# Kernel optimization log

Hardware: AMD Instinct MI355X
Metric: run time of the kernel (lower is better)

## Reference

```python
import jax, jax.numpy as jnp
import numpy as np

N = 170000          # n_users + n_entities
NNZ = 2720000       # edges in sparse A_in (avg degree 16)
DIMS = [64, 64, 32, 16]
NEG_SLOPE = 0.01    # nn.LeakyReLU default
EPS = 1e-12         # F.normalize eps


def setup_inputs() -> dict:
    key = jax.random.key(0)
    ks = jax.random.split(key, 20)
    inp = {
        "embeddings": jax.random.normal(ks[0], (N, DIMS[0]), jnp.float32) * 0.1,
        "a_vals": jax.random.uniform(ks[1], (NNZ,), jnp.float32) / 16.0,  # ~row-normalized
    }
    # bi-interaction layer params, stored (in, out) so y = x @ W + b
    i = 2
    for l in range(3):
        din, dout = DIMS[l], DIMS[l + 1]
        s = 1.0 / np.sqrt(din)
        inp[f"w1_{l}"] = jax.random.normal(ks[i], (din, dout), jnp.float32) * s; i += 1
        inp[f"b1_{l}"] = jnp.zeros((dout,), jnp.float32)
        inp[f"w2_{l}"] = jax.random.normal(ks[i], (din, dout), jnp.float32) * s; i += 1
        inp[f"b2_{l}"] = jnp.zeros((dout,), jnp.float32)
    inp["a_rows"] = jax.random.randint(ks[i], (NNZ,), 0, N, jnp.int32); i += 1
    inp["a_cols"] = jax.random.randint(ks[i], (NNZ,), 0, N, jnp.int32)
    return inp


def _leaky(x):
    return jnp.where(x >= 0, x, NEG_SLOPE * x)


def _l2norm(x):
    n = jnp.sqrt(jnp.sum(x * x, axis=1, keepdims=True))
    return x / jnp.maximum(n, EPS)


def _spmm(vals, rows, cols, emb):
    # sparse A (COO) @ emb : gather source rows, scale, scatter-add to dest rows
    msgs = vals[:, None] * emb[cols]          # (nnz, d)
    return jax.ops.segment_sum(msgs, rows, num_segments=N)


def reference(embeddings, a_vals,
              w1_0, b1_0, w2_0, b2_0,
              w1_1, b1_1, w2_1, b2_1,
              w1_2, b1_2, w2_2, b2_2,
              a_rows, a_cols):
    layers = [(w1_0, b1_0, w2_0, b2_0),
              (w1_1, b1_1, w2_1, b2_1),
              (w1_2, b1_2, w2_2, b2_2)]
    ego = embeddings
    all_embed = [ego]
    for (w1, b1, w2, b2) in layers:
        side = _spmm(a_vals, a_rows, a_cols, ego)            # (N, d_in)
        sum_e = _leaky((ego + side) @ w1 + b1)               # bi-interaction
        bi_e = _leaky((ego * side) @ w2 + b2)
        ego = sum_e + bi_e                                   # dropout = identity (eval)
        all_embed.append(_l2norm(ego))
    return jnp.concatenate(all_embed, axis=1)                # (N, 176)
```

## Files before the change

### kernel.cpp

```cpp
#include <hip/hip_runtime.h>
#include <hip/hip_bf16.h>

#define NEG_SLOPE 0.01f
#define L2EPS 1e-12f
#define SCAN_CHUNK 2048
#define PART_CH 8192
#define BSHIFT 9

__device__ __forceinline__ unsigned short f2bf(float f) {
    unsigned u = __float_as_uint(f);
    return (unsigned short)((u + 0x7fffu + ((u >> 16) & 1u)) >> 16);
}


__global__ void scan_sum(const int* __restrict__ counts, int* __restrict__ partials, int n) {
    __shared__ int red[256];
    int base = blockIdx.x * SCAN_CHUNK;
    int s = 0;
    for (int i = threadIdx.x; i < SCAN_CHUNK; i += 256) {
        int idx = base + i;
        s += (idx < n) ? counts[idx] : 0;
    }
    red[threadIdx.x] = s; __syncthreads();
    for (int o = 128; o > 0; o >>= 1) {
        if (threadIdx.x < o) red[threadIdx.x] += red[threadIdx.x + o];
        __syncthreads();
    }
    if (threadIdx.x == 0) partials[blockIdx.x] = red[0];
}

__global__ void scan_partials(int* __restrict__ partials, int nb, int* __restrict__ out, int n) {
    if (threadIdx.x == 0 && blockIdx.x == 0) {
        int run = 0;
        for (int i = 0; i < nb; i++) { int v = partials[i]; partials[i] = run; run += v; }
        out[n] = run;
    }
}

__global__ void scan_apply(const int* __restrict__ counts, const int* __restrict__ partials,
                           int* __restrict__ out, int n) {
    __shared__ int lsum[256];
    int base = blockIdx.x * SCAN_CHUNK;
    int t = threadIdx.x;
    int my[8];
    int s = 0;
    int tb = base + t * 8;
    for (int i = 0; i < 8; i++) { int idx = tb + i; int v = (idx < n) ? counts[idx] : 0; my[i] = v; s += v; }
    lsum[t] = s; __syncthreads();
    for (int o = 1; o < 256; o <<= 1) {
        int v = (t >= o) ? lsum[t - o] : 0;
        __syncthreads();
        lsum[t] += v;
        __syncthreads();
    }
    int excl = lsum[t] - s + partials[blockIdx.x];
    for (int i = 0; i < 8; i++) {
        int idx = tb + i;
        if (idx < n) { out[idx] = excl; excl += my[i]; }
    }
}


__global__ void part_hist(const int* __restrict__ rows, int* __restrict__ hist,
                          int nnz, int nchunks, int B) {
    __shared__ int h[512];
    int c = blockIdx.x;
    for (int i = threadIdx.x; i < B; i += 256) h[i] = 0;
    __syncthreads();
    int s = c * PART_CH, e = min(s + PART_CH, nnz);
    for (int i = s + threadIdx.x; i < e; i += 256) atomicAdd(&h[rows[i] >> BSHIFT], 1);
    __syncthreads();
    for (int b = threadIdx.x; b < B; b += 256) hist[b * nchunks + c] = h[b];
}

__global__ void part_scatter(const int* __restrict__ rows, const int* __restrict__ cols,
                             const float* __restrict__ vals, const int* __restrict__ hscan,
                             int2* __restrict__ tmp, int nnz, int nchunks, int B) {
    __shared__ int cur[512];
    int c = blockIdx.x;
    for (int b = threadIdx.x; b < B; b += 256) cur[b] = hscan[b * nchunks + c];
    __syncthreads();
    int s = c * PART_CH, e = min(s + PART_CH, nnz);
    for (int i = s + threadIdx.x; i < e; i += 256) {
        int r = rows[i];
        int p = atomicAdd(&cur[r >> BSHIFT], 1);
        tmp[p] = make_int2(((r & 511) << 18) | cols[i], __float_as_int(vals[i]));
    }
}

__global__ void bucket_scatter(const int* __restrict__ hscan, const int2* __restrict__ tmp,
                               int2* __restrict__ pedge, int* __restrict__ offsets,
                               int nnz, int nchunks, int B, int n) {
    __shared__ int cnt[512];
    __shared__ int scn[256];
    int b = blockIdx.x;
    int t = threadIdx.x;
    int rbase = b << BSHIFT;
    cnt[t] = 0; cnt[t + 256] = 0;
    __syncthreads();
    int s = hscan[b * nchunks];
    int e = (b == B - 1) ? nnz : hscan[(b + 1) * nchunks];
    for (int j = s + t; j < e; j += 256) atomicAdd(&cnt[((unsigned)tmp[j].x) >> 18], 1);
    __syncthreads();
    int c0 = cnt[2 * t], c1 = cnt[2 * t + 1];
    int ssum = c0 + c1;
    scn[t] = ssum;
    __syncthreads();
    for (int o = 1; o < 256; o <<= 1) {
        int v = (t >= o) ? scn[t - o] : 0;
        __syncthreads();
        scn[t] += v;
        __syncthreads();
    }
    int excl = scn[t] - ssum + s;
    int g0 = rbase + 2 * t, g1 = g0 + 1;
    if (g0 < n) offsets[g0] = excl;
    if (g1 < n) offsets[g1] = excl + c0;
    cnt[2 * t] = excl;
    cnt[2 * t + 1] = excl + c0;
    if (b == B - 1 && t == 0) offsets[n] = nnz;
    __syncthreads();
    for (int j = s + t; j < e; j += 256) {
        int2 tt = tmp[j];
        int r9 = ((unsigned)tt.x) >> 18;
        int p = atomicAdd(&cnt[r9], 1);
        pedge[p] = make_int2(tt.x & 0x3FFFF, tt.y);
    }
}


__global__ void to_bf16(const float* __restrict__ src, unsigned short* __restrict__ dst, int n4) {
    int i = blockIdx.x * blockDim.x + threadIdx.x;
    if (i >= n4) return;
    float4 v = ((const float4*)src)[i];
    ushort4 o;
    o.x = f2bf(v.x); o.y = f2bf(v.y); o.z = f2bf(v.z); o.w = f2bf(v.w);
    ((ushort4*)dst)[i] = o;
}


template <int D>
__global__ void spmm_kernel(const unsigned short* __restrict__ egob, const int* __restrict__ offs,
                            const int2* __restrict__ pedge, float* __restrict__ side, int nrows) {
    constexpr int LANES = D / 8;
    int gid = blockIdx.x * blockDim.x + threadIdx.x;
    int row = gid / LANES;
    int lane = gid % LANES;
    if (row >= nrows) return;
    int j0 = offs[row], j1 = offs[row + 1];
    float acc[8] = {0.f, 0.f, 0.f, 0.f, 0.f, 0.f, 0.f, 0.f};
    for (int j = j0; j < j1; ++j) {
        int2 ed = pedge[j];
        float v = __int_as_float(ed.y);
        uint4 q = ((const uint4*)(egob + (size_t)ed.x * D))[lane];
        acc[0] += v * __uint_as_float(q.x << 16);
        acc[1] += v * __uint_as_float(q.x & 0xffff0000u);
        acc[2] += v * __uint_as_float(q.y << 16);
        acc[3] += v * __uint_as_float(q.y & 0xffff0000u);
        acc[4] += v * __uint_as_float(q.z << 16);
        acc[5] += v * __uint_as_float(q.z & 0xffff0000u);
        acc[6] += v * __uint_as_float(q.w << 16);
        acc[7] += v * __uint_as_float(q.w & 0xffff0000u);
    }
    float4* sp = (float4*)(side + (size_t)row * D + lane * 8);
    sp[0] = make_float4(acc[0], acc[1], acc[2], acc[3]);
    sp[1] = make_float4(acc[4], acc[5], acc[6], acc[7]);
}


__device__ __forceinline__ float leaky1(float x) { return x >= 0.f ? x : NEG_SLOPE * x; }

template <int DIN, int DOUT>
__global__ void dense_kernel(const float* __restrict__ ego, const float* __restrict__ side,
                             const float* __restrict__ w1, const float* __restrict__ b1,
                             const float* __restrict__ w2, const float* __restrict__ b2,
                             float* __restrict__ ego_next, unsigned short* __restrict__ egob_next,
                             float* __restrict__ outp, int col_off, int nrows) {
    constexpr int RPB = 64;
    constexpr int TX = DOUT / 4;
    constexpr int TY = 16;
    constexpr int NT = TX * TY;
    constexpr int LD4 = DIN / 4;
    constexpr int RPP = NT / LD4;

    __shared__ float sU[DIN][RPB + 4];
    __shared__ float sV[DIN][RPB + 4];
    __shared__ float sW1[DIN * DOUT];
    __shared__ float sW2[DIN * DOUT];

    int tid = threadIdx.x;
    int row0 = blockIdx.x * RPB;

    for (int i = tid; i < DIN * DOUT / 4; i += NT) {
        ((float4*)sW1)[i] = ((const float4*)w1)[i];
        ((float4*)sW2)[i] = ((const float4*)w2)[i];
    }
    {
        int kq = tid % LD4, rr = tid / LD4;
        for (int r = rr; r < RPB; r += RPP) {
            int g = row0 + r;
            if (g < nrows) {
                float4 e = ((const float4*)(ego + (size_t)g * DIN))[kq];
                float4 s = ((const float4*)(side + (size_t)g * DIN))[kq];
                sU[kq * 4 + 0][r] = e.x + s.x;
                sU[kq * 4 + 1][r] = e.y + s.y;
                sU[kq * 4 + 2][r] = e.z + s.z;
                sU[kq * 4 + 3][r] = e.w + s.w;
                sV[kq * 4 + 0][r] = e.x * s.x;
                sV[kq * 4 + 1][r] = e.y * s.y;
                sV[kq * 4 + 2][r] = e.z * s.z;
                sV[kq * 4 + 3][r] = e.w * s.w;
            }
        }
    }
    __syncthreads();

    int tx = tid % TX, ty = tid / TX;
    float4 a1[4], a2[4];
#pragma unroll
    for (int i = 0; i < 4; i++) {
        a1[i] = make_float4(0.f, 0.f, 0.f, 0.f);
        a2[i] = make_float4(0.f, 0.f, 0.f, 0.f);
    }

#pragma unroll 8
    for (int k = 0; k < DIN; k++) {
        float4 w1v = *(const float4*)&sW1[k * DOUT + tx * 4];
        float4 w2v = *(const float4*)&sW2[k * DOUT + tx * 4];
        float4 uv = *(const float4*)&sU[k][ty * 4];
        float4 vv = *(const float4*)&sV[k][ty * 4];
        a1[0].x += uv.x * w1v.x; a1[0].y += uv.x * w1v.y; a1[0].z += uv.x * w1v.z; a1[0].w += uv.x * w1v.w;
        a1[1].x += uv.y * w1v.x; a1[1].y += uv.y * w1v.y; a1[1].z += uv.y * w1v.z; a1[1].w += uv.y * w1v.w;
        a1[2].x += uv.z * w1v.x; a1[2].y += uv.z * w1v.y; a1[2].z += uv.z * w1v.z; a1[2].w += uv.z * w1v.w;
        a1[3].x += uv.w * w1v.x; a1[3].y += uv.w * w1v.y; a1[3].z += uv.w * w1v.z; a1[3].w += uv.w * w1v.w;
        a2[0].x += vv.x * w2v.x; a2[0].y += vv.x * w2v.y; a2[0].z += vv.x * w2v.z; a2[0].w += vv.x * w2v.w;
        a2[1].x += vv.y * w2v.x; a2[1].y += vv.y * w2v.y; a2[1].z += vv.y * w2v.z; a2[1].w += vv.y * w2v.w;
        a2[2].x += vv.z * w2v.x; a2[2].y += vv.z * w2v.y; a2[2].z += vv.z * w2v.z; a2[2].w += vv.z * w2v.w;
        a2[3].x += vv.w * w2v.x; a2[3].y += vv.w * w2v.y; a2[3].z += vv.w * w2v.z; a2[3].w += vv.w * w2v.w;
    }

    float4 bb1 = ((const float4*)b1)[tx];
    float4 bb2 = ((const float4*)b2)[tx];
#pragma unroll
    for (int i = 0; i < 4; i++) {
        int g = row0 + ty * 4 + i;
        float4 x;
        x.x = leaky1(a1[i].x + bb1.x) + leaky1(a2[i].x + bb2.x);
        x.y = leaky1(a1[i].y + bb1.y) + leaky1(a2[i].y + bb2.y);
        x.z = leaky1(a1[i].z + bb1.z) + leaky1(a2[i].z + bb2.z);
        x.w = leaky1(a1[i].w + bb1.w) + leaky1(a2[i].w + bb2.w);
        float ss = x.x * x.x + x.y * x.y + x.z * x.z + x.w * x.w;
#pragma unroll
        for (int o = TX >> 1; o > 0; o >>= 1) ss += __shfl_xor(ss, o, 64);
        if (g < nrows) {
            if (ego_next) {
                ((float4*)(ego_next + (size_t)g * DOUT))[tx] = x;
                ushort4 xb;
                xb.x = f2bf(x.x); xb.y = f2bf(x.y); xb.z = f2bf(x.z); xb.w = f2bf(x.w);
                ((ushort4*)(egob_next + (size_t)g * DOUT))[tx] = xb;
            }
            float inv = 1.f / fmaxf(sqrtf(ss), L2EPS);
            float4 y = make_float4(x.x * inv, x.y * inv, x.z * inv, x.w * inv);
            ((float4*)(outp + (size_t)g * 176 + col_off))[tx] = y;
        }
    }
}


__global__ void copy_embed(const float* __restrict__ emb, float* __restrict__ outp, int nrows) {
    int idx = blockIdx.x * blockDim.x + threadIdx.x;
    int total = nrows * 16;
    if (idx >= total) return;
    int row = idx >> 4, c = idx & 15;
    float4 v = ((const float4*)emb)[idx];
    ((float4*)(outp + (size_t)row * 176))[c] = v;
}

extern "C" void kernel_launch(void* const* d_in, const int* in_sizes, int n_in,
                              void* d_out, int out_size, void* d_ws, size_t ws_size,
                              hipStream_t stream) {
    const float* emb   = (const float*)d_in[0];
    const float* avals = (const float*)d_in[1];
    const float* w1_0 = (const float*)d_in[2];  const float* b1_0 = (const float*)d_in[3];
    const float* w2_0 = (const float*)d_in[4];  const float* b2_0 = (const float*)d_in[5];
    const float* w1_1 = (const float*)d_in[6];  const float* b1_1 = (const float*)d_in[7];
    const float* w2_1 = (const float*)d_in[8];  const float* b2_1 = (const float*)d_in[9];
    const float* w1_2 = (const float*)d_in[10]; const float* b1_2 = (const float*)d_in[11];
    const float* w2_2 = (const float*)d_in[12]; const float* b2_2 = (const float*)d_in[13];
    const int* arows = (const int*)d_in[14];
    const int* acols = (const int*)d_in[15];
    float* outp = (float*)d_out;

    const int N   = in_sizes[0] / 64;
    const int NNZ = in_sizes[14];

    const int B       = (N + 511) >> BSHIFT;
    const int nchunks = (NNZ + PART_CH - 1) / PART_CH;
    const int NH      = B * nchunks;

    char* w = (char*)d_ws;
    size_t off = 0;
    auto carve = [&](size_t bytes) { char* p = w + off; off += (bytes + 255) & ~(size_t)255; return p; };
    int*   offsets  = (int*)  carve((size_t)(N + 1) * 4);
    int*   partials = (int*)  carve(1024);
    int*   hist     = (int*)  carve((size_t)(NH + 1) * 4);
    int*   hscan    = (int*)  carve((size_t)(NH + 1) * 4);
    int2*  pedge    = (int2*) carve((size_t)NNZ * 8);
    float* side     = (float*)carve((size_t)N * 64 * 4);
    float* ego1     = (float*)carve((size_t)N * 64 * 4);
    float* ego2     = (float*)carve((size_t)N * 32 * 4);
    unsigned short* egob = (unsigned short*)carve((size_t)N * 64 * 2);
    int2*  tmp      = (int2*)side;

    const int NB2 = (NH + SCAN_CHUNK - 1) / SCAN_CHUNK;

    part_hist<<<nchunks, 256, 0, stream>>>(arows, hist, NNZ, nchunks, B);
    scan_sum<<<NB2, 256, 0, stream>>>(hist, partials, NH);
    scan_partials<<<1, 64, 0, stream>>>(partials, NB2, hscan, NH);
    scan_apply<<<NB2, 256, 0, stream>>>(hist, partials, hscan, NH);
    part_scatter<<<nchunks, 256, 0, stream>>>(arows, acols, avals, hscan, tmp, NNZ, nchunks, B);
    bucket_scatter<<<B, 256, 0, stream>>>(hscan, tmp, pedge, offsets, NNZ, nchunks, B, N);

    to_bf16<<<(N * 16 + 255) / 256, 256, 0, stream>>>(emb, egob, N * 16);
    copy_embed<<<(N * 16 + 255) / 256, 256, 0, stream>>>(emb, outp, N);

    const int DB = (N + 63) / 64;

    spmm_kernel<64><<<((size_t)N * 8 + 255) / 256, 256, 0, stream>>>(egob, offsets, pedge, side, N);
    dense_kernel<64, 64><<<DB, 256, 0, stream>>>(emb, side, w1_0, b1_0, w2_0, b2_0, ego1, egob, outp, 64, N);
    spmm_kernel<64><<<((size_t)N * 8 + 255) / 256, 256, 0, stream>>>(egob, offsets, pedge, side, N);
    dense_kernel<64, 32><<<DB, 128, 0, stream>>>(ego1, side, w1_1, b1_1, w2_1, b2_1, ego2, egob, outp, 128, N);
    spmm_kernel<32><<<((size_t)N * 4 + 255) / 256, 256, 0, stream>>>(egob, offsets, pedge, side, N);
    dense_kernel<32, 16><<<DB, 64, 0, stream>>>(ego2, side, w1_2, b1_2, w2_2, b2_2, nullptr, nullptr, outp, 160, N);
}
```

Baseline: 662.7 us.

## Fuse SpMM gather into dense bi-interaction layer kernel with ping-pong bf16 buffers

Each layer's sparse gather-accumulate now happens inside the dense kernel: four threads per row gather bf16 neighbor rows into registers, then write ego+side and ego*side straight into shared memory. This removes the fp32 side buffer's global write and read and three kernel launches. The bf16 copy and the embedding output copy are merged into one prep kernel, and weights are read from global or cache instead of being staged in shared memory. Two bf16 buffers alternate between layers so a layer never overwrites rows it is still reading. The trade-off is that gather parallelism drops to 256 threads per 64-row block, and load imbalance across rows can stall the GEMM phase.

```diff
diff --git a/kernel.cpp b/kernel.cpp
--- a/kernel.cpp
+++ b/kernel.cpp
@@ -129,121 +129,145 @@
 }
 
 
-__global__ void to_bf16(const float* __restrict__ src, unsigned short* __restrict__ dst, int n4) {
-    int i = blockIdx.x * blockDim.x + threadIdx.x;
-    if (i >= n4) return;
-    float4 v = ((const float4*)src)[i];
+__global__ void embed_prep(const float* __restrict__ emb, unsigned short* __restrict__ egob,
+                           float* __restrict__ outp, int nrows) {
+    int idx = blockIdx.x * blockDim.x + threadIdx.x;
+    if (idx >= nrows * 16) return;
+    int row = idx >> 4, c = idx & 15;
+    float4 v = ((const float4*)emb)[idx];
+    ((float4*)(outp + (size_t)row * 176))[c] = v;
     ushort4 o;
     o.x = f2bf(v.x); o.y = f2bf(v.y); o.z = f2bf(v.z); o.w = f2bf(v.w);
-    ((ushort4*)dst)[i] = o;
-}
-
-
-template <int D>
-__global__ void spmm_kernel(const unsigned short* __restrict__ egob, const int* __restrict__ offs,
-                            const int2* __restrict__ pedge, float* __restrict__ side, int nrows) {
-    constexpr int LANES = D / 8;
-    int gid = blockIdx.x * blockDim.x + threadIdx.x;
-    int row = gid / LANES;
-    int lane = gid % LANES;
-    if (row >= nrows) return;
-    int j0 = offs[row], j1 = offs[row + 1];
-    float acc[8] = {0.f, 0.f, 0.f, 0.f, 0.f, 0.f, 0.f, 0.f};
-    for (int j = j0; j < j1; ++j) {
-        int2 ed = pedge[j];
-        float v = __int_as_float(ed.y);
-        uint4 q = ((const uint4*)(egob + (size_t)ed.x * D))[lane];
-        acc[0] += v * __uint_as_float(q.x << 16);
-        acc[1] += v * __uint_as_float(q.x & 0xffff0000u);
-        acc[2] += v * __uint_as_float(q.y << 16);
-        acc[3] += v * __uint_as_float(q.y & 0xffff0000u);
-        acc[4] += v * __uint_as_float(q.z << 16);
-        acc[5] += v * __uint_as_float(q.z & 0xffff0000u);
-        acc[6] += v * __uint_as_float(q.w << 16);
-        acc[7] += v * __uint_as_float(q.w & 0xffff0000u);
-    }
-    float4* sp = (float4*)(side + (size_t)row * D + lane * 8);
-    sp[0] = make_float4(acc[0], acc[1], acc[2], acc[3]);
-    sp[1] = make_float4(acc[4], acc[5], acc[6], acc[7]);
+    ((ushort4*)egob)[idx] = o;
 }
 
 
 __device__ __forceinline__ float leaky1(float x) { return x >= 0.f ? x : NEG_SLOPE * x; }
 
+__device__ __forceinline__ void fma8(float v, uint4 qv, float* acc) {
+    acc[0] += v * __uint_as_float(qv.x << 16);
+    acc[1] += v * __uint_as_float(qv.x & 0xffff0000u);
+    acc[2] += v * __uint_as_float(qv.y << 16);
+    acc[3] += v * __uint_as_float(qv.y & 0xffff0000u);
+    acc[4] += v * __uint_as_float(qv.z << 16);
+    acc[5] += v * __uint_as_float(qv.z & 0xffff0000u);
+    acc[6] += v * __uint_as_float(qv.w << 16);
+    acc[7] += v * __uint_as_float(qv.w & 0xffff0000u);
+}
+
 template <int DIN, int DOUT>
-__global__ void dense_kernel(const float* __restrict__ ego, const float* __restrict__ side,
-                             const float* __restrict__ w1, const float* __restrict__ b1,
-                             const float* __restrict__ w2, const float* __restrict__ b2,
-                             float* __restrict__ ego_next, unsigned short* __restrict__ egob_next,
-                             float* __restrict__ outp, int col_off, int nrows) {
+__global__ __launch_bounds__(256, 4)
+void fused_layer(const unsigned short* __restrict__ egob, const int* __restrict__ offs,
+                 const int2* __restrict__ pedge, const float* __restrict__ ego,
+                 const float* __restrict__ w1, const float* __restrict__ b1,
+                 const float* __restrict__ w2, const float* __restrict__ b2,
+                 float* __restrict__ ego_next, unsigned short* __restrict__ egob_next,
+                 float* __restrict__ outp, int col_off, int nrows) {
     constexpr int RPB = 64;
-    constexpr int TX = DOUT / 4;
-    constexpr int TY = 16;
-    constexpr int NT = TX * TY;
-    constexpr int LD4 = DIN / 4;
-    constexpr int RPP = NT / LD4;
+    constexpr int CPL = DIN / 4;
+    constexpr int U4  = CPL / 8;
+    constexpr int TX  = DOUT / 4;
+    constexpr int TY  = 256 / TX;
+    constexpr int RPT = RPB / TY;
 
     __shared__ float sU[DIN][RPB + 4];
     __shared__ float sV[DIN][RPB + 4];
-    __shared__ float sW1[DIN * DOUT];
-    __shared__ float sW2[DIN * DOUT];
 
     int tid = threadIdx.x;
     int row0 = blockIdx.x * RPB;
 
-    for (int i = tid; i < DIN * DOUT / 4; i += NT) {
-        ((float4*)sW1)[i] = ((const float4*)w1)[i];
-        ((float4*)sW2)[i] = ((const float4*)w2)[i];
-    }
     {
-        int kq = tid % LD4, rr = tid / LD4;
-        for (int r = rr; r < RPB; r += RPP) {
-            int g = row0 + r;
-            if (g < nrows) {
-                float4 e = ((const float4*)(ego + (size_t)g * DIN))[kq];
-                float4 s = ((const float4*)(side + (size_t)g * DIN))[kq];
-                sU[kq * 4 + 0][r] = e.x + s.x;
-                sU[kq * 4 + 1][r] = e.y + s.y;
-                sU[kq * 4 + 2][r] = e.z + s.z;
-                sU[kq * 4 + 3][r] = e.w + s.w;
-                sV[kq * 4 + 0][r] = e.x * s.x;
-                sV[kq * 4 + 1][r] = e.y * s.y;
-                sV[kq * 4 + 2][r] = e.z * s.z;
-                sV[kq * 4 + 3][r] = e.w * s.w;
+        int r = tid >> 2, q = tid & 3;
+        int g = row0 + r;
+        float acc[CPL];
+#pragma unroll
+        for (int i = 0; i < CPL; i++) acc[i] = 0.f;
+        if (g < nrows) {
+            int j0 = offs[g], j1 = offs[g + 1];
+            int j = j0;
+            for (; j + 1 < j1; j += 2) {
+                int2 e0 = pedge[j];
+                int2 e1 = pedge[j + 1];
+                float v0 = __int_as_float(e0.y);
+                float v1 = __int_as_float(e1.y);
+                const uint4* s0 = (const uint4*)(egob + (size_t)e0.x * DIN) + q * U4;
+                const uint4* s1 = (const uint4*)(egob + (size_t)e1.x * DIN) + q * U4;
+                uint4 qa[U4], qb[U4];
+#pragma unroll
+                for (int u = 0; u < U4; u++) qa[u] = s0[u];
+#pragma unroll
+                for (int u = 0; u < U4; u++) qb[u] = s1[u];
+#pragma unroll
+                for (int u = 0; u < U4; u++) fma8(v0, qa[u], acc + u * 8);
+#pragma unroll
+                for (int u = 0; u < U4; u++) fma8(v1, qb[u], acc + u * 8);
             }
+            if (j < j1) {
+                int2 e0 = pedge[j];
+                float v0 = __int_as_float(e0.y);
+                const uint4* s0 = (const uint4*)(egob + (size_t)e0.x * DIN) + q * U4;
+                uint4 qa[U4];
+#pragma unroll
+                for (int u = 0; u < U4; u++) qa[u] = s0[u];
+#pragma unroll
+                for (int u = 0; u < U4; u++) fma8(v0, qa[u], acc + u * 8);
+            }
+            const float4* ep = (const float4*)(ego + (size_t)g * DIN) + q * (CPL / 4);
+#pragma unroll
+            for (int i = 0; i < CPL / 4; i++) {
+                float4 e = ep[i];
+                int k0 = q * CPL + i * 4;
+                sU[k0 + 0][r] = e.x + acc[i * 4 + 0]; sV[k0 + 0][r] = e.x * acc[i * 4 + 0];
+                sU[k0 + 1][r] = e.y + acc[i * 4 + 1]; sV[k0 + 1][r] = e.y * acc[i * 4 + 1];
+                sU[k0 + 2][r] = e.z + acc[i * 4 + 2]; sV[k0 + 2][r] = e.z * acc[i * 4 + 2];
+                sU[k0 + 3][r] = e.w + acc[i * 4 + 3]; sV[k0 + 3][r] = e.w * acc[i * 4 + 3];
+            }
+        } else {
+#pragma unroll
+            for (int i = 0; i < CPL; i++) { sU[q * CPL + i][r] = 0.f; sV[q * CPL + i][r] = 0.f; }
         }
     }
     __syncthreads();
 
     int tx = tid % TX, ty = tid / TX;
-    float4 a1[4], a2[4];
-#pragma unroll
-    for (int i = 0; i < 4; i++) {
+    float4 a1[RPT], a2[RPT];
+#pragma unroll
+    for (int i = 0; i < RPT; i++) {
         a1[i] = make_float4(0.f, 0.f, 0.f, 0.f);
         a2[i] = make_float4(0.f, 0.f, 0.f, 0.f);
     }
 
 #pragma unroll 8
     for (int k = 0; k < DIN; k++) {
-        float4 w1v = *(const float4*)&sW1[k * DOUT + tx * 4];
-        float4 w2v = *(const float4*)&sW2[k * DOUT + tx * 4];
-        float4 uv = *(const float4*)&sU[k][ty * 4];
-        float4 vv = *(const float4*)&sV[k][ty * 4];
-        a1[0].x += uv.x * w1v.x; a1[0].y += uv.x * w1v.y; a1[0].z += uv.x * w1v.z; a1[0].w += uv.x * w1v.w;
-        a1[1].x += uv.y * w1v.x; a1[1].y += uv.y * w1v.y; a1[1].z += uv.y * w1v.z; a1[1].w += uv.y * w1v.w;
-        a1[2].x += uv.z * w1v.x; a1[2].y += uv.z * w1v.y; a1[2].z += uv.z * w1v.z; a1[2].w += uv.z * w1v.w;
-        a1[3].x += uv.w * w1v.x; a1[3].y += uv.w * w1v.y; a1[3].z += uv.w * w1v.z; a1[3].w += uv.w * w1v.w;
-        a2[0].x += vv.x * w2v.x; a2[0].y += vv.x * w2v.y; a2[0].z += vv.x * w2v.z; a2[0].w += vv.x * w2v.w;
-        a2[1].x += vv.y * w2v.x; a2[1].y += vv.y * w2v.y; a2[1].z += vv.y * w2v.z; a2[1].w += vv.y * w2v.w;
-        a2[2].x += vv.z * w2v.x; a2[2].y += vv.z * w2v.y; a2[2].z += vv.z * w2v.z; a2[2].w += vv.z * w2v.w;
-        a2[3].x += vv.w * w2v.x; a2[3].y += vv.w * w2v.y; a2[3].z += vv.w * w2v.z; a2[3].w += vv.w * w2v.w;
+        float4 w1v = ((const float4*)w1)[k * TX + tx];
+        float4 w2v = ((const float4*)w2)[k * TX + tx];
+        float uv[RPT], vv[RPT];
+        if constexpr (RPT == 4) {
+            float4 t1 = *(const float4*)&sU[k][ty * 4];
+            float4 t2 = *(const float4*)&sV[k][ty * 4];
+            uv[0] = t1.x; uv[1] = t1.y; uv[2] = t1.z; uv[3] = t1.w;
+            vv[0] = t2.x; vv[1] = t2.y; vv[2] = t2.z; vv[3] = t2.w;
+        } else if constexpr (RPT == 2) {
+            float2 t1 = *(const float2*)&sU[k][ty * 2];
+            float2 t2 = *(const float2*)&sV[k][ty * 2];
+            uv[0] = t1.x; uv[1] = t1.y;
+            vv[0] = t2.x; vv[1] = t2.y;
+        } else {
+            uv[0] = sU[k][ty];
+            vv[0] = sV[k][ty];
+        }
+#pragma unroll
+        for (int i = 0; i < RPT; i++) {
+            a1[i].x += uv[i] * w1v.x; a1[i].y += uv[i] * w1v.y; a1[i].z += uv[i] * w1v.z; a1[i].w += uv[i] * w1v.w;
+            a2[i].x += vv[i] * w2v.x; a2[i].y += vv[i] * w2v.y; a2[i].z += vv[i] * w2v.z; a2[i].w += vv[i] * w2v.w;
+        }
     }
 
     float4 bb1 = ((const float4*)b1)[tx];
     float4 bb2 = ((const float4*)b2)[tx];
 #pragma unroll
-    for (int i = 0; i < 4; i++) {
-        int g = row0 + ty * 4 + i;
+    for (int i = 0; i < RPT; i++) {
+        int g = row0 + ty * RPT + i;
         float4 x;
         x.x = leaky1(a1[i].x + bb1.x) + leaky1(a2[i].x + bb2.x);
         x.y = leaky1(a1[i].y + bb1.y) + leaky1(a2[i].y + bb2.y);
@@ -264,16 +288,6 @@
             ((float4*)(outp + (size_t)g * 176 + col_off))[tx] = y;
         }
     }
-}
-
-
-__global__ void copy_embed(const float* __restrict__ emb, float* __restrict__ outp, int nrows) {
-    int idx = blockIdx.x * blockDim.x + threadIdx.x;
-    int total = nrows * 16;
-    if (idx >= total) return;
-    int row = idx >> 4, c = idx & 15;
-    float4 v = ((const float4*)emb)[idx];
-    ((float4*)(outp + (size_t)row * 176))[c] = v;
 }
 
 extern "C" void kernel_launch(void* const* d_in, const int* in_sizes, int n_in,
@@ -306,11 +320,11 @@
     int*   hist     = (int*)  carve((size_t)(NH + 1) * 4);
     int*   hscan    = (int*)  carve((size_t)(NH + 1) * 4);
     int2*  pedge    = (int2*) carve((size_t)NNZ * 8);
-    float* side     = (float*)carve((size_t)N * 64 * 4);
     float* ego1     = (float*)carve((size_t)N * 64 * 4);
     float* ego2     = (float*)carve((size_t)N * 32 * 4);
-    unsigned short* egob = (unsigned short*)carve((size_t)N * 64 * 2);
-    int2*  tmp      = (int2*)side;
+    unsigned short* egobA = (unsigned short*)carve((size_t)N * 64 * 2);
+    unsigned short* egobB = (unsigned short*)carve((size_t)N * 64 * 2);
+    int2*  tmp      = (int2*)ego1;
 
     const int NB2 = (NH + SCAN_CHUNK - 1) / SCAN_CHUNK;
 
@@ -321,15 +335,17 @@
     part_scatter<<<nchunks, 256, 0, stream>>>(arows, acols, avals, hscan, tmp, NNZ, nchunks, B);
     bucket_scatter<<<B, 256, 0, stream>>>(hscan, tmp, pedge, offsets, NNZ, nchunks, B, N);
 
-    to_bf16<<<(N * 16 + 255) / 256, 256, 0, stream>>>(emb, egob, N * 16);
-    copy_embed<<<(N * 16 + 255) / 256, 256, 0, stream>>>(emb, outp, N);
+    embed_prep<<<(N * 16 + 255) / 256, 256, 0, stream>>>(emb, egobA, outp, N);
 
     const int DB = (N + 63) / 64;
 
-    spmm_kernel<64><<<((size_t)N * 8 + 255) / 256, 256, 0, stream>>>(egob, offsets, pedge, side, N);
-    dense_kernel<64, 64><<<DB, 256, 0, stream>>>(emb, side, w1_0, b1_0, w2_0, b2_0, ego1, egob, outp, 64, N);
-    spmm_kernel<64><<<((size_t)N * 8 + 255) / 256, 256, 0, stream>>>(egob, offsets, pedge, side, N);
-    dense_kernel<64, 32><<<DB, 128, 0, stream>>>(ego1, side, w1_1, b1_1, w2_1, b2_1, ego2, egob, outp, 128, N);
-    spmm_kernel<32><<<((size_t)N * 4 + 255) / 256, 256, 0, stream>>>(egob, offsets, pedge, side, N);
-    dense_kernel<32, 16><<<DB, 64, 0, stream>>>(ego2, side, w1_2, b1_2, w2_2, b2_2, nullptr, nullptr, outp, 160, N);
-}
+    fused_layer<64, 64><<<DB, 256, 0, stream>>>(egobA, offsets, pedge, emb,
+                                                w1_0, b1_0, w2_0, b2_0,
+                                                ego1, egobB, outp, 64, N);
+    fused_layer<64, 32><<<DB, 256, 0, stream>>>(egobB, offsets, pedge, ego1,
+                                                w1_1, b1_1, w2_1, b2_1,
+                                                ego2, egobA, outp, 128, N);
+    fused_layer<32, 16><<<DB, 256, 0, stream>>>(egobA, offsets, pedge, ego2,
+                                                w1_2, b1_2, w2_2, b2_2,
+                                                nullptr, nullptr, outp, 160, N);
+}
```

Result: faster. 618.6 us (-6.7%).
